# Optimization experiments

Measured on AMD Instinct MI355X. Metric: run time of the kernel, lower is better.

Reference implementation:

```python
import jax, jax.numpy as jnp
import numpy as np

B, S, IN_DIM, CTX = 32, 512, 256, 128
D, H, L = 128, 4, 2
DH = D // H
HID = 512
TOTAL = 11 * D * D + 8 * D  # hypernet flat weight size per sample
EPS = 1e-5


def _layernorm(x, g, b):
    mu = jnp.mean(x, axis=-1, keepdims=True)
    var = jnp.mean(jnp.square(x - mu), axis=-1, keepdims=True)
    return (x - mu) * jax.lax.rsqrt(var + EPS) * g + b


def setup_inputs() -> dict:
    key = jax.random.key(0)
    ks = jax.random.split(key, 24)
    f32 = jnp.float32
    inp = {
        'x': jax.random.normal(ks[0], (B, S, IN_DIM), f32),
        'context_vector': jax.random.normal(ks[1], (B, CTX), f32),
        'in_proj_w': jax.random.normal(ks[2], (D, IN_DIM), f32) * (IN_DIM ** -0.5),
        'in_proj_b': jnp.zeros((D,), f32),
        'pe': jax.random.normal(ks[3], (1, S, D), f32) * 0.02,
        'hfc1_w': jax.random.normal(ks[4], (L, HID, CTX), f32) * (CTX ** -0.5),
        'hfc1_b': jnp.zeros((L, HID), f32),
        'hfc2_w': jax.random.normal(ks[5], (L, TOTAL, HID), f32) * 0.02,
        'hfc2_b': jnp.zeros((L, TOTAL), f32),
        'out_proj_w': jax.random.normal(ks[6], (L, D, D), f32) * (D ** -0.5),
        'out_proj_b': jnp.zeros((L, D), f32),
        'ln1_g': jnp.ones((L, D), f32), 'ln1_b': jnp.zeros((L, D), f32),
        'ln2_g': jnp.ones((L, D), f32), 'ln2_b': jnp.zeros((L, D), f32),
        'alpha1': jnp.full((L,), 0.5, f32), 'alpha2': jnp.full((L,), 0.5, f32),
        'head_w': jax.random.normal(ks[7], (1, D), f32) * (D ** -0.5),
        'head_b': jnp.zeros((1,), f32),
    }
    return inp


def reference(x, context_vector, in_proj_w, in_proj_b, pe, hfc1_w, hfc1_b,
              hfc2_w, hfc2_b, out_proj_w, out_proj_b, ln1_g, ln1_b,
              ln2_g, ln2_b, alpha1, alpha2, head_w, head_b):
    # input projection + learned positional encoding
    h = jnp.einsum('bsi,di->bsd', x, in_proj_w) + in_proj_b
    h = h + pe[:, :h.shape[1], :]

    # flat split offsets for hypernet output
    sizes = [3 * D * D, 3 * D, 4 * D * D, 4 * D, 4 * D * D, D]
    offs = np.concatenate([[0], np.cumsum(sizes)])

    for l in range(L):
        # hypernet: per-sample weights from context
        hid = jax.nn.relu(context_vector @ hfc1_w[l].T + hfc1_b[l])
        flat = hid @ hfc2_w[l].T + hfc2_b[l]  # [B, TOTAL]
        aw = flat[:, offs[0]:offs[1]].reshape(B, 3 * D, D)
        ab = flat[:, offs[1]:offs[2]]                     # [B, 3D]
        f1w = flat[:, offs[2]:offs[3]].reshape(B, 4 * D, D)
        f1b = flat[:, offs[3]:offs[4]]                    # [B, 4D]
        f2w = flat[:, offs[4]:offs[5]].reshape(B, D, 4 * D)
        f2b = flat[:, offs[5]:offs[6]]                    # [B, D]

        # per-sample QKV projection (grouped GEMM over batch)
        qkv = jnp.einsum('bsd,bed->bse', h, aw) + ab[:, None, :]
        q, k, v = jnp.split(qkv, 3, axis=-1)
        q = q.reshape(B, S, H, DH)
        k = k.reshape(B, S, H, DH)
        v = v.reshape(B, S, H, DH)
        scores = jnp.einsum('bqhd,bkhd->bhqk', q, k) / jnp.sqrt(jnp.float32(DH))
        attn = jax.nn.softmax(scores, axis=-1)
        ctx = jnp.einsum('bhqk,bkhd->bqhd', attn, v).reshape(B, S, D)
        attn_out = jnp.einsum('bsd,ed->bse', ctx, out_proj_w[l]) + out_proj_b[l]

        h = _layernorm(h + alpha1[l] * attn_out, ln1_g[l], ln1_b[l])

        # per-sample FFN
        ff = jax.nn.relu(jnp.einsum('bsd,bfd->bsf', h, f1w) + f1b[:, None, :])
        ff = jnp.einsum('bsf,bdf->bsd', ff, f2w) + f2b[:, None, :]

        h = _layernorm(h + alpha2[l] * ff, ln2_g[l], ln2_b[l])

    out = h[:, -1, :] @ head_w.T + head_b  # [B, 1]
    return out
```

## Files before the change

### kernel.cpp

```cpp
#include <hip/hip_runtime.h>
#include <hip/hip_bf16.h>

constexpr int B_    = 32;
constexpr int S_    = 512;
constexpr int INDIM = 256;
constexpr int KCTX  = 128;
constexpr int D_    = 128;
constexpr int H_    = 4;
constexpr int L_    = 2;
constexpr int HID_  = 512;
constexpr int TOTAL_ = 11 * D_ * D_ + 8 * D_;
constexpr int OFF_AB  = 3 * D_ * D_;
constexpr int OFF_F1W = OFF_AB + 3 * D_;
constexpr int OFF_F1B = OFF_F1W + 4 * D_ * D_;
constexpr int OFF_F2W = OFF_F1B + 4 * D_;
constexpr int OFF_F2B = OFF_F2W + 4 * D_ * D_;
constexpr int TP = 132;

typedef __attribute__((ext_vector_type(8))) short short8;
typedef __attribute__((ext_vector_type(4))) short short4v;
typedef __attribute__((ext_vector_type(2))) short short2v;
typedef __attribute__((ext_vector_type(4))) float f32x4;

#define MFMA16 __builtin_amdgcn_mfma_f32_16x16x32_bf16

__device__ __forceinline__ short f2bf(float f) {
  __hip_bfloat16 h = __float2bfloat16(f);
  return __builtin_bit_cast(short, h);
}
__device__ __forceinline__ float bf2f(short s) {
  __hip_bfloat16 h = __builtin_bit_cast(__hip_bfloat16, s);
  return __bfloat162float(h);
}
struct bfpair { short hi, lo; };
__device__ __forceinline__ bfpair split2p(float x) {
  bfpair p;
  p.hi = f2bf(x);
  p.lo = f2bf(x - bf2f(p.hi));
  return p;
}

__device__ __forceinline__ long ftaddr(int row, int k, int K) {
  return ((long)(row >> 4) * (K >> 3) + (k >> 3)) * 128 + (row & 15) * 8 + (k & 7);
}

__global__ void k_cvtft(const float* __restrict__ in, short* __restrict__ oh,
                        short* __restrict__ ol, int ktShift, int n8) {
  int t = blockIdx.x * 256 + threadIdx.x;
  if (t >= n8) return;
  int kt = 1 << ktShift;
  int row = t >> ktShift;
  int kc = t & (kt - 1);
  const float* p = in + ((long)row << (ktShift + 3)) + kc * 8;
  float4 v0 = *(const float4*)p;
  float4 v1 = *(const float4*)(p + 4);
  short8 h8, l8;
  bfpair q;
  q = split2p(v0.x); h8[0] = q.hi; l8[0] = q.lo;
  q = split2p(v0.y); h8[1] = q.hi; l8[1] = q.lo;
  q = split2p(v0.z); h8[2] = q.hi; l8[2] = q.lo;
  q = split2p(v0.w); h8[3] = q.hi; l8[3] = q.lo;
  q = split2p(v1.x); h8[4] = q.hi; l8[4] = q.lo;
  q = split2p(v1.y); h8[5] = q.hi; l8[5] = q.lo;
  q = split2p(v1.z); h8[6] = q.hi; l8[6] = q.lo;
  q = split2p(v1.w); h8[7] = q.hi; l8[7] = q.lo;
  long o = ((long)(row >> 4) * kt + kc) * 128 + (row & 15) * 8;
  *(short8*)(oh + o) = h8;
  *(short8*)(ol + o) = l8;
}

__global__ __launch_bounds__(512) void k_hid(const float* __restrict__ cvec,
                                             const float* __restrict__ w,
                                             const float* __restrict__ bias,
                                             short* __restrict__ hh,
                                             short* __restrict__ hl) {
  int lb = blockIdx.x;
  int b  = lb & 31;
  int j  = threadIdx.x;
  __shared__ float cs[KCTX];
  if (j < KCTX) cs[j] = cvec[b * KCTX + j];
  __syncthreads();
  int l = lb >> 5;
  const float* wr = w + (long)(l * HID_ + j) * KCTX;
  float s = bias[l * HID_ + j];
  #pragma unroll
  for (int c = 0; c < KCTX; c += 4) {
    float4 cv = *(const float4*)(cs + c);
    float4 wv = *(const float4*)(wr + c);
    s += cv.x * wv.x + cv.y * wv.y + cv.z * wv.z + cv.w * wv.w;
  }
  s = fmaxf(s, 0.f);
  bfpair p = split2p(s);
  long o = (long)l * 32 * HID_ + ((long)(b >> 4) * 64 + (j >> 3)) * 128 + (b & 15) * 8 + (j & 7);
  hh[o] = p.hi;
  hl[o] = p.lo;
}

__device__ __forceinline__ void store_flat(int b, int trow, float v,
    short* __restrict__ awh, short* __restrict__ awl,
    short* __restrict__ f1h, short* __restrict__ f1l,
    short* __restrict__ f2h, short* __restrict__ f2l,
    float* __restrict__ ab, float* __restrict__ f1b, float* __restrict__ f2b) {
  if (trow < OFF_AB) {
    int e = trow >> 7, d = trow & 127;
    long a = (long)b * 49152 + ftaddr(e, d, 128);
    bfpair p = split2p(v); awh[a] = p.hi; awl[a] = p.lo;
  } else if (trow < OFF_F1W) {
    ab[b * 384 + trow - OFF_AB] = v;
  } else if (trow < OFF_F1B) {
    int i = trow - OFF_F1W; int f = i >> 7, d = i & 127;
    long a = (long)b * 65536 + ftaddr(f, d, 128);
    bfpair p = split2p(v); f1h[a] = p.hi; f1l[a] = p.lo;
  } else if (trow < OFF_F2W) {
    f1b[b * 512 + trow - OFF_F1B] = v;
  } else if (trow < OFF_F2B) {
    int i = trow - OFF_F2W; int dd = i >> 9, f = i & 511;
    long a = (long)b * 65536 + ftaddr(dd, f, 512);
    bfpair p = split2p(v); f2h[a] = p.hi; f2l[a] = p.lo;
  } else {
    f2b[b * 128 + trow - OFF_F2B] = v;
  }
}

__global__ __launch_bounds__(256) void k_flat(
    const short* __restrict__ hidh, const short* __restrict__ hidl,
    const float* __restrict__ W, const float* __restrict__ bias,
    short* __restrict__ awh, short* __restrict__ awl,
    short* __restrict__ f1h, short* __restrict__ f1l,
    short* __restrict__ f2h, short* __restrict__ f2l,
    float* __restrict__ ab, float* __restrict__ f1b, float* __restrict__ f2b) {
  __shared__ short wls[2][64 * 64];
  const int l = blockIdx.y;
  hidh += (long)l * 32 * HID_;
  hidl += (long)l * 32 * HID_;
  W    += (long)l * TOTAL_ * HID_;
  bias += (long)l * TOTAL_;
  awh  += (long)l * B_ * 49152;  awl += (long)l * B_ * 49152;
  f1h  += (long)l * B_ * 65536;  f1l += (long)l * B_ * 65536;
  f2h  += (long)l * B_ * 65536;  f2l += (long)l * B_ * 65536;
  ab   += l * B_ * 384;  f1b += l * B_ * 512;  f2b += l * B_ * 128;
  const int tid = threadIdx.x, wave = tid >> 6, lane = tid & 63;
  const int r = lane & 15, g = lane >> 4;
  const int nb0 = blockIdx.x * 64;
  const int rr = tid >> 4;
  const int cc = (tid & 15) * 4;
  const float* wbase = W + (long)nb0 * HID_;
  float4 wv[2][4];
  #pragma unroll
  for (int rnd = 0; rnd < 4; ++rnd) {
    wv[0][rnd] = *(const float4*)(wbase + (long)(rnd * 16 + rr) * HID_ + cc);
    wv[1][rnd] = *(const float4*)(wbase + (long)(rnd * 16 + rr) * HID_ + 64 + cc);
  }
  const short* pAh = hidh + g * 128 + r * 8;
  const short* pAl = hidl + g * 128 + r * 8;
  f32x4 acc0 = {0, 0, 0, 0}, acc1 = {0, 0, 0, 0};
  int cur = 0;
  for (int c0 = 0; c0 < 512; c0 += 64) {
    #pragma unroll
    for (int rnd = 0; rnd < 4; ++rnd) {
      int row = rnd * 16 + rr;
      short4v h4, l4; bfpair q;
      q = split2p(wv[cur][rnd].x); h4[0] = q.hi; l4[0] = q.lo;
      q = split2p(wv[cur][rnd].y); h4[1] = q.hi; l4[1] = q.lo;
      q = split2p(wv[cur][rnd].z); h4[2] = q.hi; l4[2] = q.lo;
      q = split2p(wv[cur][rnd].w); h4[3] = q.hi; l4[3] = q.lo;
      int sb = row * 128 + ((cc * 2) ^ ((row & 7) << 4));
      *(short4v*)((char*)&wls[0][0] + sb) = h4;
      *(short4v*)((char*)&wls[1][0] + sb) = l4;
    }
    if (c0 + 128 < 512) {
      #pragma unroll
      for (int rnd = 0; rnd < 4; ++rnd)
        wv[cur][rnd] = *(const float4*)(wbase + (long)(rnd * 16 + rr) * HID_ + (c0 + 128) + cc);
    }
    __syncthreads();
    #pragma unroll
    for (int kk = 0; kk < 2; ++kk) {
      long ao = (long)(c0 * 16) + kk * 512;
      short8 ah0 = *(const short8*)(pAh + ao);
      short8 ah1 = *(const short8*)(pAh + 8192 + ao);
      short8 al0 = *(const short8*)(pAl + ao);
      short8 al1 = *(const short8*)(pAl + 8192 + ao);
      int wrow = wave * 16 + r;
      int wb = wrow * 128 + ((kk * 64 + g * 16) ^ ((r & 7) << 4));
      short8 wh = *(const short8*)((char*)&wls[0][0] + wb);
      short8 wl = *(const short8*)((char*)&wls[1][0] + wb);
      acc0 = MFMA16(ah0, wl, acc0, 0, 0, 0);
      acc0 = MFMA16(al0, wh, acc0, 0, 0, 0);
      acc0 = MFMA16(ah0, wh, acc0, 0, 0, 0);
      acc1 = MFMA16(ah1, wl, acc1, 0, 0, 0);
      acc1 = MFMA16(al1, wh, acc1, 0, 0, 0);
      acc1 = MFMA16(ah1, wh, acc1, 0, 0, 0);
    }
    __syncthreads();
    cur ^= 1;
  }
  int trow = nb0 + wave * 16 + r;
  float bv = bias[trow];
  #pragma unroll
  for (int reg = 0; reg < 4; ++reg) {
    store_flat(g * 4 + reg, trow, acc0[reg] + bv, awh, awl, f1h, f1l, f2h, f2l, ab, f1b, f2b);
    store_flat(g * 4 + reg + 16, trow, acc1[reg] + bv, awh, awl, f1h, f1l, f2h, f2l, ab, f1b, f2b);
  }
}

template <int K, int EPI, bool RELU>
__global__ __launch_bounds__(256) void k_gemm(
    const short* __restrict__ Ah, const short* __restrict__ Al, long sA,
    const short* __restrict__ Wh, const short* __restrict__ Wl, long sW,
    const float* __restrict__ biasP, long sB,
    void* __restrict__ p0, void* __restrict__ p1,
    void* __restrict__ p2, void* __restrict__ p3,
    const float* __restrict__ pe, int N,
    const float* __restrict__ lng, const float* __restrict__ lnb,
    const float* __restrict__ lnal) {
  extern __shared__ char smem_dyn[];
  const int tid = threadIdx.x, wave = tid >> 6, lane = tid & 63;
  const int r = lane & 15, g = lane >> 4;
  const int b = blockIdx.z;
  const int m0 = blockIdx.x * 64 + (wave & 1) * 32;
  const int n0 = blockIdx.y * 128 + (wave >> 1) * 64;
  const long KT = (long)K * 16;
  const short* pAh = Ah + (long)b * sA + (m0 >> 4) * KT + g * 128 + r * 8;
  const short* pAl = Al + (long)b * sA + (m0 >> 4) * KT + g * 128 + r * 8;
  const short* pWh = Wh + (long)b * sW + (n0 >> 4) * KT + g * 128 + r * 8;
  const short* pWl = Wl + (long)b * sW + (n0 >> 4) * KT + g * 128 + r * 8;
  f32x4 acc[2][4] = {{{0,0,0,0},{0,0,0,0},{0,0,0,0},{0,0,0,0}},
                     {{0,0,0,0},{0,0,0,0},{0,0,0,0},{0,0,0,0}}};
  for (int kk = 0; kk < K / 32; ++kk) {
    long ko = (long)kk * 512;
    short8 a0h = *(const short8*)(pAh + ko);
    short8 a1h = *(const short8*)(pAh + KT + ko);
    short8 a0l = *(const short8*)(pAl + ko);
    short8 a1l = *(const short8*)(pAl + KT + ko);
    #pragma unroll
    for (int ns = 0; ns < 4; ++ns) {
      short8 wh = *(const short8*)(pWh + ns * KT + ko);
      short8 wl = *(const short8*)(pWl + ns * KT + ko);
      acc[0][ns] = MFMA16(a0h, wl, acc[0][ns], 0, 0, 0);
      acc[0][ns] = MFMA16(a0l, wh, acc[0][ns], 0, 0, 0);
      acc[0][ns] = MFMA16(a0h, wh, acc[0][ns], 0, 0, 0);
      acc[1][ns] = MFMA16(a1h, wl, acc[1][ns], 0, 0, 0);
      acc[1][ns] = MFMA16(a1l, wh, acc[1][ns], 0, 0, 0);
      acc[1][ns] = MFMA16(a1h, wh, acc[1][ns], 0, 0, 0);
    }
  }

  if constexpr (EPI == 5) {
    if (blockIdx.y == 2) {
      #pragma unroll
      for (int ms = 0; ms < 2; ++ms) {
        int crow0 = m0 + ms * 16 + g * 4;
        #pragma unroll
        for (int ns = 0; ns < 4; ++ns) {
          int ccol = n0 + ns * 16 + r;
          float bv = biasP[(long)b * sB + ccol];
          int c2 = ccol - 256, hd = c2 >> 5, dd = c2 & 31;
          short4v h4, l4; bfpair q;
          #pragma unroll
          for (int reg = 0; reg < 4; ++reg) {
            float v = acc[ms][ns][reg] + bv;
            q = split2p(v); h4[reg] = q.hi; l4[reg] = q.lo;
          }
          long o = (long)(b * 4 + hd) * 16384 + (dd >> 4) * 8192
                 + (crow0 >> 3) * 128 + (dd & 15) * 8 + (crow0 & 7);
          *(short4v*)((short*)p2 + o) = h4;
          *(short4v*)((short*)p3 + o) = l4;
        }
      }
      return;
    }
  }

  if constexpr (EPI == 1) {
    #pragma unroll
    for (int ms = 0; ms < 2; ++ms) {
      #pragma unroll
      for (int ns = 0; ns < 4; ++ns) {
        int ccol = n0 + ns * 16 + r;
        float bv = biasP[ccol];
        #pragma unroll
        for (int reg = 0; reg < 4; ++reg) {
          int crow = m0 + ms * 16 + g * 4 + reg;
          float v = acc[ms][ns][reg] + bv + pe[crow * D_ + ccol];
          ((float*)p0)[((long)b * S_ + crow) * D_ + ccol] = v;
          long o = (long)b * 65536 + (long)(crow >> 4) * 2048
                 + (ccol >> 3) * 128 + (crow & 15) * 8 + (ccol & 7);
          bfpair sp = split2p(v);
          ((short*)p1)[o] = sp.hi;
          ((short*)p2)[o] = sp.lo;
        }
      }
    }
    return;
  }

  float* tile = (float*)smem_dyn;
  #pragma unroll
  for (int ms = 0; ms < 2; ++ms) {
    #pragma unroll
    for (int ns = 0; ns < 4; ++ns) {
      int ccol = n0 + ns * 16 + r;
      float bv = biasP[(long)b * sB + ccol];
      #pragma unroll
      for (int reg = 0; reg < 4; ++reg) {
        float v = acc[ms][ns][reg] + bv;
        if constexpr (RELU) v = fmaxf(v, 0.f);
        int trow2 = (wave & 1) * 32 + ms * 16 + g * 4 + reg;
        int tcol = (wave >> 1) * 64 + ns * 16 + r;
        tile[trow2 * TP + tcol] = v;
      }
    }
  }
  __syncthreads();

  if constexpr (EPI == 0 || EPI == 5) {
    int row = tid >> 2, cg = tid & 3;
    int crow = blockIdx.x * 64 + row;
    long rowbase = (long)b * 512 * N + (long)(crow >> 4) * (16 * (long)N) + (crow & 15) * 8;
    #pragma unroll
    for (int j4 = 0; j4 < 4; ++j4) {
      int tcol = j4 * 32 + cg * 8;
      float4 aa = *(const float4*)&tile[row * TP + tcol];
      float4 bb = *(const float4*)&tile[row * TP + tcol + 4];
      short8 h8, l8; bfpair q;
      q = split2p(aa.x); h8[0] = q.hi; l8[0] = q.lo;
      q = split2p(aa.y); h8[1] = q.hi; l8[1] = q.lo;
      q = split2p(aa.z); h8[2] = q.hi; l8[2] = q.lo;
      q = split2p(aa.w); h8[3] = q.hi; l8[3] = q.lo;
      q = split2p(bb.x); h8[4] = q.hi; l8[4] = q.lo;
      q = split2p(bb.y); h8[5] = q.hi; l8[5] = q.lo;
      q = split2p(bb.z); h8[6] = q.hi; l8[6] = q.lo;
      q = split2p(bb.w); h8[7] = q.hi; l8[7] = q.lo;
      int ccol = blockIdx.y * 128 + tcol;
      long o = rowbase + (long)(ccol >> 3) * 128;
      *(short8*)((short*)p0 + o) = h8;
      *(short8*)((short*)p1 + o) = l8;
    }
  } else if constexpr (EPI == 4) {
    int row = tid >> 2, q = tid & 3;
    int brow = blockIdx.x * 64 + row;
    float a = lnal[0];
    float* hf = (float*)p0;
    float* hrow = hf + ((long)b * S_ + brow) * D_ + q * 32;
    float tv[32];
    float s = 0.f, ss = 0.f;
    #pragma unroll
    for (int i = 0; i < 32; i += 4) {
      float4 hv = *(const float4*)(hrow + i);
      float4 yv = *(const float4*)&tile[row * TP + q * 32 + i];
      float t0 = hv.x + a * yv.x, t1 = hv.y + a * yv.y;
      float t2 = hv.z + a * yv.z, t3 = hv.w + a * yv.w;
      tv[i] = t0; tv[i+1] = t1; tv[i+2] = t2; tv[i+3] = t3;
      s += t0 + t1 + t2 + t3;
      ss += t0*t0 + t1*t1 + t2*t2 + t3*t3;
    }
    s  += __shfl_xor(s, 1);  s  += __shfl_xor(s, 2);
    ss += __shfl_xor(ss, 1); ss += __shfl_xor(ss, 2);
    float mu = s * (1.f / 128.f);
    float varv = ss * (1.f / 128.f) - mu * mu;
    float inv = rsqrtf(varv + 1e-5f);
    short* ph = (short*)p1; short* pl = (short*)p2;
    long fb = (long)b * 65536 + (long)(brow >> 4) * 2048 + (brow & 15) * 8;
    #pragma unroll
    for (int j = 0; j < 4; ++j) {
      short8 hv8, lv8;
      #pragma unroll
      for (int e = 0; e < 8; e += 4) {
        int i = j * 8 + e;
        int c = q * 32 + i;
        float4 gv = *(const float4*)(lng + c);
        float4 bb = *(const float4*)(lnb + c);
        float4 o4;
        o4.x = (tv[i]   - mu) * inv * gv.x + bb.x;
        o4.y = (tv[i+1] - mu) * inv * gv.y + bb.y;
        o4.z = (tv[i+2] - mu) * inv * gv.z + bb.z;
        o4.w = (tv[i+3] - mu) * inv * gv.w + bb.w;
        *(float4*)(hrow + i) = o4;
        bfpair q0 = split2p(o4.x); hv8[e]   = q0.hi; lv8[e]   = q0.lo;
        bfpair q1 = split2p(o4.y); hv8[e+1] = q1.hi; lv8[e+1] = q1.lo;
        bfpair q2 = split2p(o4.z); hv8[e+2] = q2.hi; lv8[e+2] = q2.lo;
        bfpair q3 = split2p(o4.w); hv8[e+3] = q3.hi; lv8[e+3] = q3.lo;
      }
      long o = fb + (q * 4 + j) * 128;
      *(short8*)(ph + o) = hv8;
      *(short8*)(pl + o) = lv8;
    }
  }
}

__global__ __launch_bounds__(128) void k_attn(const short* __restrict__ qkh,
                                              const short* __restrict__ qkl,
                                              const short* __restrict__ vth,
                                              const short* __restrict__ vtl,
                                              short* __restrict__ ch,
                                              short* __restrict__ cl) {
  __shared__ __align__(16) float scr[16][516];
  __shared__ __align__(16) float obuf[16][34];
  const int tid = threadIdx.x, wave = tid >> 6, lane = tid & 63;
  const int r = lane & 15, g = lane >> 4;
  const int b = blockIdx.z, hh = blockIdx.y;
  const int m0 = blockIdx.x * 16;
  const long qb = (long)b * 131072;
  const long qoff = qb + (long)(m0 >> 4) * 4096 + (hh * 4 + g) * 128 + r * 8;
  short8 qh = *(const short8*)(qkh + qoff);
  short8 ql = *(const short8*)(qkl + qoff);
  const float sc = 0.17677669529663687f;
  for (int n0 = wave * 256; n0 < wave * 256 + 256; n0 += 16) {
    long koff = qb + (long)(n0 >> 4) * 4096 + (16 + hh * 4 + g) * 128 + r * 8;
    short8 kh = *(const short8*)(qkh + koff);
    short8 kl = *(const short8*)(qkl + koff);
    f32x4 s = {0, 0, 0, 0};
    s = MFMA16(qh, kl, s, 0, 0, 0);
    s = MFMA16(ql, kh, s, 0, 0, 0);
    s = MFMA16(qh, kh, s, 0, 0, 0);
    #pragma unroll
    for (int reg = 0; reg < 4; ++reg)
      scr[g * 4 + reg][n0 + r] = s[reg] * sc;
  }
  __syncthreads();
  for (int row = wave * 8; row < wave * 8 + 8; ++row) {
    float v[8];
    #pragma unroll
    for (int i = 0; i < 8; ++i) v[i] = scr[row][lane + i * 64];
    float m = v[0];
    #pragma unroll
    for (int i = 1; i < 8; ++i) m = fmaxf(m, v[i]);
    #pragma unroll
    for (int o = 32; o > 0; o >>= 1) m = fmaxf(m, __shfl_xor(m, o));
    float ssum = 0.f;
    #pragma unroll
    for (int i = 0; i < 8; ++i) { v[i] = __expf(v[i] - m); ssum += v[i]; }
    #pragma unroll
    for (int o = 32; o > 0; o >>= 1) ssum += __shfl_xor(ssum, o);
    float inv = 1.f / ssum;
    #pragma unroll
    for (int i = 0; i < 8; ++i) scr[row][lane + i * 64] = v[i] * inv;
  }
  __syncthreads();
  f32x4 o0 = {0, 0, 0, 0}, o1 = {0, 0, 0, 0};
  const long vb = (long)(b * 4 + hh) * 16384;
  for (int kt = wave * 8; kt < wave * 8 + 8; ++kt) {
    float4 pv0 = *(const float4*)&scr[r][kt * 32 + g * 8];
    float4 pv1 = *(const float4*)&scr[r][kt * 32 + g * 8 + 4];
    short8 pah, pal;
    bfpair p;
    p = split2p(pv0.x); pah[0] = p.hi; pal[0] = p.lo;
    p = split2p(pv0.y); pah[1] = p.hi; pal[1] = p.lo;
    p = split2p(pv0.z); pah[2] = p.hi; pal[2] = p.lo;
    p = split2p(pv0.w); pah[3] = p.hi; pal[3] = p.lo;
    p = split2p(pv1.x); pah[4] = p.hi; pal[4] = p.lo;
    p = split2p(pv1.y); pah[5] = p.hi; pal[5] = p.lo;
    p = split2p(pv1.z); pah[6] = p.hi; pal[6] = p.lo;
    p = split2p(pv1.w); pah[7] = p.hi; pal[7] = p.lo;
    long vo = vb + (long)(kt * 4 + g) * 128 + r * 8;
    short8 vh0 = *(const short8*)(vth + vo);
    short8 vh1 = *(const short8*)(vth + vo + 8192);
    short8 vl0 = *(const short8*)(vtl + vo);
    short8 vl1 = *(const short8*)(vtl + vo + 8192);
    o0 = MFMA16(pah, vl0, o0, 0, 0, 0);
    o0 = MFMA16(pal, vh0, o0, 0, 0, 0);
    o0 = MFMA16(pah, vh0, o0, 0, 0, 0);
    o1 = MFMA16(pah, vl1, o1, 0, 0, 0);
    o1 = MFMA16(pal, vh1, o1, 0, 0, 0);
    o1 = MFMA16(pah, vh1, o1, 0, 0, 0);
  }
  if (wave == 1) {
    #pragma unroll
    for (int reg = 0; reg < 4; ++reg) {
      obuf[g * 4 + reg][r] = o0[reg];
      obuf[g * 4 + reg][17 + r] = o1[reg];
    }
  }
  __syncthreads();
  if (wave == 0) {
    #pragma unroll
    for (int reg = 0; reg < 4; ++reg) {
      float a0 = o0[reg] + obuf[g * 4 + reg][r];
      float a1 = o1[reg] + obuf[g * 4 + reg][17 + r];
      int srow = m0 + g * 4 + reg;
      int col0 = hh * 32 + r;
      long o = (long)b * 65536 + (long)(srow >> 4) * 2048
             + (col0 >> 3) * 128 + (srow & 15) * 8 + (col0 & 7);
      bfpair sp0 = split2p(a0);
      ch[o] = sp0.hi; cl[o] = sp0.lo;
      long o2 = o + 2 * 128;
      bfpair sp1 = split2p(a1);
      ch[o2] = sp1.hi; cl[o2] = sp1.lo;
    }
  }
}

__global__ __launch_bounds__(64) void k_head(const float* __restrict__ h,
                                             const float* __restrict__ hw,
                                             const float* __restrict__ hb,
                                             float* __restrict__ out) {
  int b = blockIdx.x, lane = threadIdx.x;
  const float* hr = h + ((long)b * S_ + (S_ - 1)) * D_;
  float v = hr[lane] * hw[lane] + hr[lane + 64] * hw[lane + 64];
  #pragma unroll
  for (int o = 32; o > 0; o >>= 1) v += __shfl_xor(v, o);
  if (lane == 0) out[b] = v + hb[0];
}

extern "C" void kernel_launch(void* const* d_in, const int* in_sizes, int n_in,
                              void* d_out, int out_size, void* d_ws, size_t ws_size,
                              hipStream_t stream) {
  const float* x    = (const float*)d_in[0];
  const float* cvec = (const float*)d_in[1];
  const float* ipw  = (const float*)d_in[2];
  const float* ipb  = (const float*)d_in[3];
  const float* pe   = (const float*)d_in[4];
  const float* h1w  = (const float*)d_in[5];
  const float* h1b  = (const float*)d_in[6];
  const float* h2w  = (const float*)d_in[7];
  const float* h2b  = (const float*)d_in[8];
  const float* opw  = (const float*)d_in[9];
  const float* opb  = (const float*)d_in[10];
  const float* ln1g = (const float*)d_in[11];
  const float* ln1b = (const float*)d_in[12];
  const float* ln2g = (const float*)d_in[13];
  const float* ln2b = (const float*)d_in[14];
  const float* a1   = (const float*)d_in[15];
  const float* a2   = (const float*)d_in[16];
  const float* hw   = (const float*)d_in[17];
  const float* hb   = (const float*)d_in[18];
  float* out = (float*)d_out;

  char* ws = (char*)d_ws;
  size_t off = 0;
  auto alloc = [&](size_t n) { void* p = ws + off; off = (off + n + 255) & ~(size_t)255; return p; };

  const long AWs = (long)B_ * 49152;
  const long F1s = (long)B_ * 65536;
  const long F2s = (long)B_ * 65536;

  short* ff1h  = (short*)alloc((size_t)B_ * S_ * 512 * 2);
  short* ff1l  = (short*)alloc((size_t)B_ * S_ * 512 * 2);
  short* xFh   = ff1h;
  short* xFl   = ff1l;
  float* h_f   = (float*)alloc((size_t)B_ * S_ * D_ * 4);
  short* hFh   = (short*)alloc((size_t)B_ * S_ * D_ * 2);
  short* hFl   = (short*)alloc((size_t)B_ * S_ * D_ * 2);
  short* hidFh = (short*)alloc((size_t)L_ * 32 * HID_ * 2);
  short* hidFl = (short*)alloc((size_t)L_ * 32 * HID_ * 2);
  short* awFh  = (short*)alloc((size_t)L_ * AWs * 2);
  short* awFl  = (short*)alloc((size_t)L_ * AWs * 2);
  short* f1wFh = (short*)alloc((size_t)L_ * F1s * 2);
  short* f1wFl = (short*)alloc((size_t)L_ * F1s * 2);
  short* f2wFh = (short*)alloc((size_t)L_ * F2s * 2);
  short* f2wFl = (short*)alloc((size_t)L_ * F2s * 2);
  float* abF   = (float*)alloc((size_t)L_ * B_ * 384 * 4);
  float* f1bF  = (float*)alloc((size_t)L_ * B_ * 512 * 4);
  float* f2bF  = (float*)alloc((size_t)L_ * B_ * 128 * 4);
  short* qkFh  = (short*)alloc((size_t)B_ * S_ * 256 * 2);
  short* qkFl  = (short*)alloc((size_t)B_ * S_ * 256 * 2);
  short* vtFh  = (short*)alloc((size_t)B_ * H_ * 32 * S_ * 2);
  short* vtFl  = (short*)alloc((size_t)B_ * H_ * 32 * S_ * 2);
  short* cxFh  = (short*)alloc((size_t)B_ * S_ * D_ * 2);
  short* cxFl  = (short*)alloc((size_t)B_ * S_ * D_ * 2);
  short* ipwFh = (short*)alloc((size_t)D_ * INDIM * 2);
  short* ipwFl = (short*)alloc((size_t)D_ * INDIM * 2);
  short* opwFh = (short*)alloc((size_t)L_ * D_ * D_ * 2);
  short* opwFl = (short*)alloc((size_t)L_ * D_ * D_ * 2);

  k_cvtft<<<(B_ * S_ * INDIM / 8 + 255) / 256, 256, 0, stream>>>(x, xFh, xFl, 5, B_ * S_ * INDIM / 8);
  k_cvtft<<<16, 256, 0, stream>>>(ipw, ipwFh, ipwFl, 5, D_ * INDIM / 8);
  k_cvtft<<<16, 256, 0, stream>>>(opw, opwFh, opwFl, 4, L_ * D_ * D_ / 8);

  k_hid<<<L_ * 32, 512, 0, stream>>>(cvec, h1w, h1b, hidFh, hidFl);

  k_flat<<<dim3(TOTAL_ / 64, 2), 256, 0, stream>>>(
      hidFh, hidFl, h2w, h2b, awFh, awFl, f1wFh, f1wFl, f2wFh, f2wFl,
      abF, f1bF, f2bF);

  k_gemm<INDIM, 1, false><<<dim3(8, 1, B_), 256, 0, stream>>>(
      xFh, xFl, (long)S_ * INDIM, ipwFh, ipwFl, 0, ipb, 0,
      h_f, hFh, hFl, nullptr, pe, 128, nullptr, nullptr, nullptr);

  constexpr size_t TILE_LDS = 64 * TP * 4;
  for (int l = 0; l < L_; ++l) {
    k_gemm<D_, 5, false><<<dim3(8, 3, B_), 256, TILE_LDS, stream>>>(
        hFh, hFl, (long)S_ * D_, awFh + l * AWs, awFl + l * AWs, 49152,
        abF + l * B_ * 384, 384,
        qkFh, qkFl, vtFh, vtFl, nullptr, 256, nullptr, nullptr, nullptr);
    k_attn<<<dim3(S_ / 16, H_, B_), 128, 0, stream>>>(qkFh, qkFl, vtFh, vtFl, cxFh, cxFl);
    k_gemm<D_, 4, false><<<dim3(8, 1, B_), 256, TILE_LDS, stream>>>(
        cxFh, cxFl, (long)S_ * D_, opwFh + l * 16384, opwFl + l * 16384, 0,
        opb + l * D_, 0, h_f, hFh, hFl, nullptr, nullptr, 128,
        ln1g + l * D_, ln1b + l * D_, a1 + l);
    k_gemm<D_, 0, true><<<dim3(8, 4, B_), 256, TILE_LDS, stream>>>(
        hFh, hFl, (long)S_ * D_, f1wFh + l * F1s, f1wFl + l * F1s, 65536,
        f1bF + l * B_ * 512, 512,
        ff1h, ff1l, nullptr, nullptr, nullptr, 512, nullptr, nullptr, nullptr);
    k_gemm<512, 4, false><<<dim3(8, 1, B_), 256, TILE_LDS, stream>>>(
        ff1h, ff1l, (long)S_ * 512, f2wFh + l * F2s, f2wFl + l * F2s, 65536,
        f2bF + l * B_ * 128, 128,
        h_f, hFh, hFl, nullptr, nullptr, 128,
        ln2g + l * D_, ln2b + l * D_, a2 + l);
  }
  k_head<<<B_, 64, 0, stream>>>(h_f, hw, hb, out);
}
```

Baseline: 506.1 us.

## Prune last layer to rows feeding the head and vectorize hypernet output stores

The final layer is cut down to the work that reaches the output. K and V are still computed for all positions, but attention, the output projection, the FFN and the LayerNorms run only for the last 64-row block, and attention only for the last 16 queries, since the head reads only the final token. Grid offset parameters are added to the GEMM and attention kernels so they can start at those tail blocks. Separately, the hypernet output epilogue now stages results through shared memory so each thread writes 8 contiguous values with vector stores instead of scattered scalar stores.

```diff
diff --git a/kernel.cpp b/kernel.cpp
--- a/kernel.cpp
+++ b/kernel.cpp
@@ -94,32 +94,6 @@
   long o = (long)l * 32 * HID_ + ((long)(b >> 4) * 64 + (j >> 3)) * 128 + (b & 15) * 8 + (j & 7);
   hh[o] = p.hi;
   hl[o] = p.lo;
-}
-
-__device__ __forceinline__ void store_flat(int b, int trow, float v,
-    short* __restrict__ awh, short* __restrict__ awl,
-    short* __restrict__ f1h, short* __restrict__ f1l,
-    short* __restrict__ f2h, short* __restrict__ f2l,
-    float* __restrict__ ab, float* __restrict__ f1b, float* __restrict__ f2b) {
-  if (trow < OFF_AB) {
-    int e = trow >> 7, d = trow & 127;
-    long a = (long)b * 49152 + ftaddr(e, d, 128);
-    bfpair p = split2p(v); awh[a] = p.hi; awl[a] = p.lo;
-  } else if (trow < OFF_F1W) {
-    ab[b * 384 + trow - OFF_AB] = v;
-  } else if (trow < OFF_F1B) {
-    int i = trow - OFF_F1W; int f = i >> 7, d = i & 127;
-    long a = (long)b * 65536 + ftaddr(f, d, 128);
-    bfpair p = split2p(v); f1h[a] = p.hi; f1l[a] = p.lo;
-  } else if (trow < OFF_F2W) {
-    f1b[b * 512 + trow - OFF_F1B] = v;
-  } else if (trow < OFF_F2B) {
-    int i = trow - OFF_F2W; int dd = i >> 9, f = i & 511;
-    long a = (long)b * 65536 + ftaddr(dd, f, 512);
-    bfpair p = split2p(v); f2h[a] = p.hi; f2l[a] = p.lo;
-  } else {
-    f2b[b * 128 + trow - OFF_F2B] = v;
-  }
 }
 
 __global__ __launch_bounds__(256) void k_flat(
@@ -195,12 +169,63 @@
     __syncthreads();
     cur ^= 1;
   }
-  int trow = nb0 + wave * 16 + r;
-  float bv = bias[trow];
-  #pragma unroll
-  for (int reg = 0; reg < 4; ++reg) {
-    store_flat(g * 4 + reg, trow, acc0[reg] + bv, awh, awl, f1h, f1l, f2h, f2l, ab, f1b, f2b);
-    store_flat(g * 4 + reg + 16, trow, acc1[reg] + bv, awh, awl, f1h, f1l, f2h, f2l, ab, f1b, f2b);
+  constexpr int TPF = 68;
+  float* tile = (float*)&wls[0][0];
+  {
+    int trow = nb0 + wave * 16 + r;
+    float bv = bias[trow];
+    int col = wave * 16 + r;
+    #pragma unroll
+    for (int reg = 0; reg < 4; ++reg) {
+      tile[(g * 4 + reg) * TPF + col]        = acc0[reg] + bv;
+      tile[(g * 4 + reg + 16) * TPF + col]   = acc1[reg] + bv;
+    }
+  }
+  __syncthreads();
+  {
+    int b  = tid >> 3;
+    int cg = tid & 7;
+    int t0 = nb0 + cg * 8;
+    float v[8];
+    #pragma unroll
+    for (int j = 0; j < 8; ++j) v[j] = tile[b * TPF + cg * 8 + j];
+    if (t0 < OFF_AB) {
+      int e = t0 >> 7, d = t0 & 127;
+      long a = (long)b * 49152 + ((long)(e >> 4) * 16 + (d >> 3)) * 128 + (e & 15) * 8;
+      short8 h8, l8; bfpair q;
+      #pragma unroll
+      for (int j = 0; j < 8; ++j) { q = split2p(v[j]); h8[j] = q.hi; l8[j] = q.lo; }
+      *(short8*)(awh + a) = h8;
+      *(short8*)(awl + a) = l8;
+    } else if (t0 < OFF_F1W) {
+      float* dst = ab + b * 384 + (t0 - OFF_AB);
+      float4 x0 = {v[0], v[1], v[2], v[3]}, x1 = {v[4], v[5], v[6], v[7]};
+      *(float4*)dst = x0; *(float4*)(dst + 4) = x1;
+    } else if (t0 < OFF_F1B) {
+      int i = t0 - OFF_F1W; int f = i >> 7, d = i & 127;
+      long a = (long)b * 65536 + ((long)(f >> 4) * 16 + (d >> 3)) * 128 + (f & 15) * 8;
+      short8 h8, l8; bfpair q;
+      #pragma unroll
+      for (int j = 0; j < 8; ++j) { q = split2p(v[j]); h8[j] = q.hi; l8[j] = q.lo; }
+      *(short8*)(f1h + a) = h8;
+      *(short8*)(f1l + a) = l8;
+    } else if (t0 < OFF_F2W) {
+      float* dst = f1b + b * 512 + (t0 - OFF_F1B);
+      float4 x0 = {v[0], v[1], v[2], v[3]}, x1 = {v[4], v[5], v[6], v[7]};
+      *(float4*)dst = x0; *(float4*)(dst + 4) = x1;
+    } else if (t0 < OFF_F2B) {
+      int i = t0 - OFF_F2W; int dd = i >> 9, f = i & 511;
+      long a = (long)b * 65536 + ((long)(dd >> 4) * 64 + (f >> 3)) * 128 + (dd & 15) * 8;
+      short8 h8, l8; bfpair q;
+      #pragma unroll
+      for (int j = 0; j < 8; ++j) { q = split2p(v[j]); h8[j] = q.hi; l8[j] = q.lo; }
+      *(short8*)(f2h + a) = h8;
+      *(short8*)(f2l + a) = l8;
+    } else {
+      float* dst = f2b + b * 128 + (t0 - OFF_F2B);
+      float4 x0 = {v[0], v[1], v[2], v[3]}, x1 = {v[4], v[5], v[6], v[7]};
+      *(float4*)dst = x0; *(float4*)(dst + 4) = x1;
+    }
   }
 }
 
@@ -213,13 +238,14 @@
     void* __restrict__ p2, void* __restrict__ p3,
     const float* __restrict__ pe, int N,
     const float* __restrict__ lng, const float* __restrict__ lnb,
-    const float* __restrict__ lnal) {
+    const float* __restrict__ lnal, int mOff, int nOff) {
   extern __shared__ char smem_dyn[];
   const int tid = threadIdx.x, wave = tid >> 6, lane = tid & 63;
   const int r = lane & 15, g = lane >> 4;
   const int b = blockIdx.z;
-  const int m0 = blockIdx.x * 64 + (wave & 1) * 32;
-  const int n0 = blockIdx.y * 128 + (wave >> 1) * 64;
+  const int bx = blockIdx.x + mOff, by = blockIdx.y + nOff;
+  const int m0 = bx * 64 + (wave & 1) * 32;
+  const int n0 = by * 128 + (wave >> 1) * 64;
   const long KT = (long)K * 16;
   const short* pAh = Ah + (long)b * sA + (m0 >> 4) * KT + g * 128 + r * 8;
   const short* pAl = Al + (long)b * sA + (m0 >> 4) * KT + g * 128 + r * 8;
@@ -247,7 +273,7 @@
   }
 
   if constexpr (EPI == 5) {
-    if (blockIdx.y == 2) {
+    if (by == 2) {
       #pragma unroll
       for (int ms = 0; ms < 2; ++ms) {
         int crow0 = m0 + ms * 16 + g * 4;
@@ -316,7 +342,7 @@
 
   if constexpr (EPI == 0 || EPI == 5) {
     int row = tid >> 2, cg = tid & 3;
-    int crow = blockIdx.x * 64 + row;
+    int crow = bx * 64 + row;
     long rowbase = (long)b * 512 * N + (long)(crow >> 4) * (16 * (long)N) + (crow & 15) * 8;
     #pragma unroll
     for (int j4 = 0; j4 < 4; ++j4) {
@@ -332,14 +358,14 @@
       q = split2p(bb.y); h8[5] = q.hi; l8[5] = q.lo;
       q = split2p(bb.z); h8[6] = q.hi; l8[6] = q.lo;
       q = split2p(bb.w); h8[7] = q.hi; l8[7] = q.lo;
-      int ccol = blockIdx.y * 128 + tcol;
+      int ccol = by * 128 + tcol;
       long o = rowbase + (long)(ccol >> 3) * 128;
       *(short8*)((short*)p0 + o) = h8;
       *(short8*)((short*)p1 + o) = l8;
     }
   } else if constexpr (EPI == 4) {
     int row = tid >> 2, q = tid & 3;
-    int brow = blockIdx.x * 64 + row;
+    int brow = bx * 64 + row;
     float a = lnal[0];
     float* hf = (float*)p0;
     float* hrow = hf + ((long)b * S_ + brow) * D_ + q * 32;
@@ -394,13 +420,14 @@
                                               const short* __restrict__ vth,
                                               const short* __restrict__ vtl,
                                               short* __restrict__ ch,
-                                              short* __restrict__ cl) {
+                                              short* __restrict__ cl,
+                                              int mOff) {
   __shared__ __align__(16) float scr[16][516];
   __shared__ __align__(16) float obuf[16][34];
   const int tid = threadIdx.x, wave = tid >> 6, lane = tid & 63;
   const int r = lane & 15, g = lane >> 4;
   const int b = blockIdx.z, hh = blockIdx.y;
-  const int m0 = blockIdx.x * 16;
+  const int m0 = (blockIdx.x + mOff) * 16;
   const long qb = (long)b * 131072;
   const long qoff = qb + (long)(m0 >> 4) * 4096 + (hh * 4 + g) * 128 + r * 8;
   short8 qh = *(const short8*)(qkh + qoff);
@@ -576,28 +603,56 @@
 
   k_gemm<INDIM, 1, false><<<dim3(8, 1, B_), 256, 0, stream>>>(
       xFh, xFl, (long)S_ * INDIM, ipwFh, ipwFl, 0, ipb, 0,
-      h_f, hFh, hFl, nullptr, pe, 128, nullptr, nullptr, nullptr);
+      h_f, hFh, hFl, nullptr, pe, 128, nullptr, nullptr, nullptr, 0, 0);
 
   constexpr size_t TILE_LDS = 64 * TP * 4;
-  for (int l = 0; l < L_; ++l) {
+
+  {
+    int l = 0;
     k_gemm<D_, 5, false><<<dim3(8, 3, B_), 256, TILE_LDS, stream>>>(
         hFh, hFl, (long)S_ * D_, awFh + l * AWs, awFl + l * AWs, 49152,
         abF + l * B_ * 384, 384,
-        qkFh, qkFl, vtFh, vtFl, nullptr, 256, nullptr, nullptr, nullptr);
-    k_attn<<<dim3(S_ / 16, H_, B_), 128, 0, stream>>>(qkFh, qkFl, vtFh, vtFl, cxFh, cxFl);
+        qkFh, qkFl, vtFh, vtFl, nullptr, 256, nullptr, nullptr, nullptr, 0, 0);
+    k_attn<<<dim3(S_ / 16, H_, B_), 128, 0, stream>>>(qkFh, qkFl, vtFh, vtFl, cxFh, cxFl, 0);
     k_gemm<D_, 4, false><<<dim3(8, 1, B_), 256, TILE_LDS, stream>>>(
         cxFh, cxFl, (long)S_ * D_, opwFh + l * 16384, opwFl + l * 16384, 0,
         opb + l * D_, 0, h_f, hFh, hFl, nullptr, nullptr, 128,
-        ln1g + l * D_, ln1b + l * D_, a1 + l);
+        ln1g + l * D_, ln1b + l * D_, a1 + l, 0, 0);
     k_gemm<D_, 0, true><<<dim3(8, 4, B_), 256, TILE_LDS, stream>>>(
         hFh, hFl, (long)S_ * D_, f1wFh + l * F1s, f1wFl + l * F1s, 65536,
         f1bF + l * B_ * 512, 512,
-        ff1h, ff1l, nullptr, nullptr, nullptr, 512, nullptr, nullptr, nullptr);
+        ff1h, ff1l, nullptr, nullptr, nullptr, 512, nullptr, nullptr, nullptr, 0, 0);
     k_gemm<512, 4, false><<<dim3(8, 1, B_), 256, TILE_LDS, stream>>>(
         ff1h, ff1l, (long)S_ * 512, f2wFh + l * F2s, f2wFl + l * F2s, 65536,
         f2bF + l * B_ * 128, 128,
         h_f, hFh, hFl, nullptr, nullptr, 128,
-        ln2g + l * D_, ln2b + l * D_, a2 + l);
+        ln2g + l * D_, ln2b + l * D_, a2 + l, 0, 0);
+  }
+
+  {
+    int l = 1;
+    k_gemm<D_, 5, false><<<dim3(8, 2, B_), 256, TILE_LDS, stream>>>(
+        hFh, hFl, (long)S_ * D_, awFh + l * AWs, awFl + l * AWs, 49152,
+        abF + l * B_ * 384, 384,
+        qkFh, qkFl, vtFh, vtFl, nullptr, 256, nullptr, nullptr, nullptr, 0, 1);
+    k_gemm<D_, 5, false><<<dim3(1, 1, B_), 256, TILE_LDS, stream>>>(
+        hFh, hFl, (long)S_ * D_, awFh + l * AWs, awFl + l * AWs, 49152,
+        abF + l * B_ * 384, 384,
+        qkFh, qkFl, vtFh, vtFl, nullptr, 256, nullptr, nullptr, nullptr, 7, 0);
+    k_attn<<<dim3(1, H_, B_), 128, 0, stream>>>(qkFh, qkFl, vtFh, vtFl, cxFh, cxFl, 31);
+    k_gemm<D_, 4, false><<<dim3(1, 1, B_), 256, TILE_LDS, stream>>>(
+        cxFh, cxFl, (long)S_ * D_, opwFh + l * 16384, opwFl + l * 16384, 0,
+        opb + l * D_, 0, h_f, hFh, hFl, nullptr, nullptr, 128,
+        ln1g + l * D_, ln1b + l * D_, a1 + l, 7, 0);
+    k_gemm<D_, 0, true><<<dim3(1, 4, B_), 256, TILE_LDS, stream>>>(
+        hFh, hFl, (long)S_ * D_, f1wFh + l * F1s, f1wFl + l * F1s, 65536,
+        f1bF + l * B_ * 512, 512,
+        ff1h, ff1l, nullptr, nullptr, nullptr, 512, nullptr, nullptr, nullptr, 7, 0);
+    k_gemm<512, 4, false><<<dim3(1, 1, B_), 256, TILE_LDS, stream>>>(
+        ff1h, ff1l, (long)S_ * 512, f2wFh + l * F2s, f2wFl + l * F2s, 65536,
+        f2bF + l * B_ * 128, 128,
+        h_f, hFh, hFl, nullptr, nullptr, 128,
+        ln2g + l * D_, ln2b + l * D_, a2 + l, 7, 0);
   }
   k_head<<<B_, 64, 0, stream>>>(h_f, hw, hb, out);
 }
```

After: 448.3 us. 1.13x faster.
